# Optimization experiments

Hardware: AMD Instinct MI355X
Metric: run time of the kernel (lower is better)

Reference implementation:

```python
import jax, jax.numpy as jnp
import numpy as np
from jax import lax

ALPHA = 0.02


def setup_inputs() -> dict:
    key = jax.random.key(0)
    k1, k2, k3, k4 = jax.random.split(key, 4)
    B, C, H, W = 32, 512, 64, 64
    Cr = C // 16  # reduction=16
    x = jax.random.normal(k1, (B, C, H, W), dtype=jnp.float32)
    w1 = jax.random.normal(k2, (Cr, C), dtype=jnp.float32) * 0.05  # Linear(C -> C/r), bias=False
    w2 = jax.random.normal(k3, (C, Cr), dtype=jnp.float32) * 0.05  # Linear(C/r -> C), bias=False
    wconv = jax.random.normal(k4, (1, 2, 7, 7), dtype=jnp.float32) * 0.05  # Conv2d(2,1,7,pad=3)
    return {"x": x, "w1": w1, "w2": w2, "wconv": wconv}


def _mlp(v, w1, w2):
    # shared MLP: Linear -> ReLU -> Linear (no biases)
    return jax.nn.relu(v @ w1.T) @ w2.T


def reference(x, w1, w2, wconv):
    # Channel attention: global avg and max pooling over H,W -> [B, C]
    avg = jnp.mean(x, axis=(2, 3))
    maxv = jnp.max(x, axis=(2, 3))
    mc = jax.nn.sigmoid(_mlp(avg, w1, w2) + _mlp(maxv, w1, w2))[:, :, None, None]  # [B,C,1,1]

    # Spatial attention: mean/max over channels -> [B, 2, H, W], then 7x7 conv
    xs = jnp.concatenate(
        [jnp.mean(x, axis=1, keepdims=True), jnp.max(x, axis=1, keepdims=True)], axis=1
    )
    ms = jax.nn.sigmoid(
        lax.conv_general_dilated(
            xs, wconv, window_strides=(1, 1), padding=[(3, 3), (3, 3)],
            dimension_numbers=("NCHW", "OIHW", "NCHW"),
        )
    )  # [B,1,H,W]

    # Soft gating with alpha blending, residual_scale=0 so output is x * att
    att = (1.0 - ALPHA + ALPHA * mc) * (1.0 - ALPHA + ALPHA * ms)
    return x * att
```

## Files before the change

kernel.cpp:

```cpp
#include <hip/hip_runtime.h>
#include <math.h>

#define ALPHA_F 0.02f

constexpr int Bn  = 32;
constexpr int Cn  = 512;
constexpr int CRn = 32;
constexpr int HWn = 4096;
constexpr int NCG = 8;
constexpr int NPG = 4;

__device__ __forceinline__ float sigmoidf_(float v) {
    return 1.0f / (1.0f + expf(-v));
}

__global__ __launch_bounds__(256) void k1_reduce(
    const float* __restrict__ x,
    float* __restrict__ cps, float* __restrict__ cpm,
    float* __restrict__ sps, float* __restrict__ spm)
{
    const int bid = blockIdx.x;
    const int pg  = bid & 3;
    const int cg  = (bid >> 2) & 7;
    const int b   = bid >> 5;
    const int t    = threadIdx.x;
    const int wv   = t >> 6;
    const int lane = t & 63;

    __shared__ float ls[4][1024];
    __shared__ float lm[4][1024];

    const float* xb = x + ((size_t)b * Cn + (size_t)cg * 64) * HWn + pg * 1024;

    float4 psum[4], pmax[4];
#pragma unroll
    for (int q = 0; q < 4; ++q) {
        psum[q] = make_float4(0.f, 0.f, 0.f, 0.f);
        pmax[q] = make_float4(-INFINITY, -INFINITY, -INFINITY, -INFINITY);
    }

#pragma unroll 4
    for (int cl = 0; cl < 16; ++cl) {
        const int c = wv * 16 + cl;
        const float4* row = (const float4*)(xb + (size_t)c * HWn);
        float lsum = 0.f, lmax = -INFINITY;
#pragma unroll
        for (int q = 0; q < 4; ++q) {
            const float4 v = row[q * 64 + lane];
            psum[q].x += v.x; psum[q].y += v.y; psum[q].z += v.z; psum[q].w += v.w;
            pmax[q].x = fmaxf(pmax[q].x, v.x);
            pmax[q].y = fmaxf(pmax[q].y, v.y);
            pmax[q].z = fmaxf(pmax[q].z, v.z);
            pmax[q].w = fmaxf(pmax[q].w, v.w);
            lsum += (v.x + v.y) + (v.z + v.w);
            lmax = fmaxf(lmax, fmaxf(fmaxf(v.x, v.y), fmaxf(v.z, v.w)));
        }
#pragma unroll
        for (int m = 32; m >= 1; m >>= 1) {
            lsum += __shfl_xor(lsum, m, 64);
            lmax = fmaxf(lmax, __shfl_xor(lmax, m, 64));
        }
        if (lane == 0) {
            const int cglob = cg * 64 + c;
            cps[(pg * Bn + b) * Cn + cglob] = lsum;
            cpm[(pg * Bn + b) * Cn + cglob] = lmax;
        }
    }

    float4* lsw = (float4*)ls[wv];
    float4* lmw = (float4*)lm[wv];
#pragma unroll
    for (int q = 0; q < 4; ++q) {
        lsw[q * 64 + lane] = psum[q];
        lmw[q * 64 + lane] = pmax[q];
    }
    __syncthreads();

    float4 s  = ((const float4*)ls[0])[t];
    float4 mx = ((const float4*)lm[0])[t];
#pragma unroll
    for (int w = 1; w < 4; ++w) {
        const float4 a  = ((const float4*)ls[w])[t];
        const float4 bb = ((const float4*)lm[w])[t];
        s.x += a.x; s.y += a.y; s.z += a.z; s.w += a.w;
        mx.x = fmaxf(mx.x, bb.x); mx.y = fmaxf(mx.y, bb.y);
        mx.z = fmaxf(mx.z, bb.z); mx.w = fmaxf(mx.w, bb.w);
    }
    float4* os = (float4*)(sps + ((size_t)cg * Bn + b) * HWn + pg * 1024);
    float4* om = (float4*)(spm + ((size_t)cg * Bn + b) * HWn + pg * 1024);
    os[t] = s;
    om[t] = mx;
}

__global__ __launch_bounds__(256) void k2_spatial_finalize(
    const float* __restrict__ sps, const float* __restrict__ spm,
    float* __restrict__ savg, float* __restrict__ smax)
{
    const int i = blockIdx.x * 256 + threadIdx.x;
    const float4* ps = (const float4*)sps;
    const float4* pm = (const float4*)spm;
    float4 s = ps[i], m = pm[i];
#pragma unroll
    for (int cg = 1; cg < NCG; ++cg) {
        const float4 a  = ps[cg * (Bn * HWn / 4) + i];
        const float4 b4 = pm[cg * (Bn * HWn / 4) + i];
        s.x += a.x; s.y += a.y; s.z += a.z; s.w += a.w;
        m.x = fmaxf(m.x, b4.x); m.y = fmaxf(m.y, b4.y);
        m.z = fmaxf(m.z, b4.z); m.w = fmaxf(m.w, b4.w);
    }
    const float inv = 1.0f / (float)Cn;
    s.x *= inv; s.y *= inv; s.z *= inv; s.w *= inv;
    ((float4*)savg)[i] = s;
    ((float4*)smax)[i] = m;
}

__global__ __launch_bounds__(256) void k2_mlp(
    const float* __restrict__ cps, const float* __restrict__ cpm,
    const float* __restrict__ w1, const float* __restrict__ w2,
    float* __restrict__ mcF)
{
    const int b = blockIdx.x;
    const int t = threadIdx.x;
    __shared__ float avg[Cn];
    __shared__ float mxv[Cn];
    __shared__ float hs[CRn];

    for (int c = t; c < Cn; c += 256) {
        float s = 0.f, m = -INFINITY;
#pragma unroll
        for (int pgi = 0; pgi < NPG; ++pgi) {
            s += cps[(pgi * Bn + b) * Cn + c];
            m = fmaxf(m, cpm[(pgi * Bn + b) * Cn + c]);
        }
        avg[c] = s * (1.0f / (float)HWn);
        mxv[c] = m;
    }
    __syncthreads();

    const int j = t >> 3, s8 = t & 7;
    float pa = 0.f, pm = 0.f;
    const float* w1r = w1 + j * Cn + s8 * 64;
    const float* av  = avg + s8 * 64;
    const float* mv  = mxv + s8 * 64;
    for (int k = 0; k < 64; ++k) {
        pa += av[k] * w1r[k];
        pm += mv[k] * w1r[k];
    }
    pa += __shfl_xor(pa, 1, 64); pm += __shfl_xor(pm, 1, 64);
    pa += __shfl_xor(pa, 2, 64); pm += __shfl_xor(pm, 2, 64);
    pa += __shfl_xor(pa, 4, 64); pm += __shfl_xor(pm, 4, 64);
    if (s8 == 0) hs[j] = fmaxf(pa, 0.f) + fmaxf(pm, 0.f);
    __syncthreads();

    for (int c = t; c < Cn; c += 256) {
        float o = 0.f;
        const float* w2r = w2 + c * CRn;
#pragma unroll
        for (int jj = 0; jj < CRn; ++jj) o += hs[jj] * w2r[jj];
        mcF[b * Cn + c] = 1.0f - ALPHA_F + ALPHA_F * sigmoidf_(o);
    }
}

__global__ __launch_bounds__(256) void k3_conv(
    const float* __restrict__ savg, const float* __restrict__ smax,
    const float* __restrict__ wconv, float* __restrict__ msF)
{
    __shared__ float wc[98];
    const int t = threadIdx.x;
    if (t < 98) wc[t] = wconv[t];
    __syncthreads();

    const int p  = blockIdx.x * 256 + t;
    const int b  = p >> 12;
    const int pl = p & 4095;
    const int y  = pl >> 6, xc = pl & 63;
    const float* sa = savg + b * HWn;
    const float* sm = smax + b * HWn;
    float acc = 0.f;
#pragma unroll
    for (int ky = 0; ky < 7; ++ky) {
        const int yy = y + ky - 3;
        if (yy < 0 || yy >= 64) continue;
#pragma unroll
        for (int kx = 0; kx < 7; ++kx) {
            const int xx = xc + kx - 3;
            if (xx < 0 || xx >= 64) continue;
            const int off = (yy << 6) + xx;
            acc += wc[ky * 7 + kx] * sa[off] + wc[49 + ky * 7 + kx] * sm[off];
        }
    }
    msF[p] = 1.0f - ALPHA_F + ALPHA_F * sigmoidf_(acc);
}

__global__ __launch_bounds__(256) void k4_apply(
    const float* __restrict__ x, const float* __restrict__ mcF,
    const float* __restrict__ msF, float* __restrict__ out)
{
    const long long N4 = (long long)Bn * Cn * HWn / 4;
    const long long stride = (long long)gridDim.x * 256;
    const float4* x4  = (const float4*)x;
    const float4* ms4 = (const float4*)msF;
    float4* o4 = (float4*)out;
    for (long long v = (long long)blockIdx.x * 256 + threadIdx.x; v < N4; v += stride) {
        const int bc = (int)(v >> 10);
        const int pq = (int)(v & 1023);
        const int b  = bc >> 9;
        const float f = mcF[bc];
        const float4 m = ms4[b * 1024 + pq];
        float4 xv = x4[v];
        xv.x *= f * m.x; xv.y *= f * m.y; xv.z *= f * m.z; xv.w *= f * m.w;
        o4[v] = xv;
    }
}

extern "C" void kernel_launch(void* const* d_in, const int* in_sizes, int n_in,
                              void* d_out, int out_size, void* d_ws, size_t ws_size,
                              hipStream_t stream)
{
    const float* x     = (const float*)d_in[0];
    const float* w1    = (const float*)d_in[1];
    const float* w2    = (const float*)d_in[2];
    const float* wconv = (const float*)d_in[3];
    float* out = (float*)d_out;

    float* p = (float*)d_ws;
    float* cps  = p; p += NPG * Bn * Cn;
    float* cpm  = p; p += NPG * Bn * Cn;
    float* sps  = p; p += NCG * Bn * HWn;
    float* spm  = p; p += NCG * Bn * HWn;
    float* savg = p; p += Bn * HWn;
    float* smax = p; p += Bn * HWn;
    float* mcF  = p; p += Bn * Cn;
    float* msF  = p; p += Bn * HWn;

    hipLaunchKernelGGL(k1_reduce, dim3(Bn * NCG * NPG), dim3(256), 0, stream,
                       x, cps, cpm, sps, spm);
    hipLaunchKernelGGL(k2_spatial_finalize, dim3(Bn * HWn / 4 / 256), dim3(256), 0, stream,
                       sps, spm, savg, smax);
    hipLaunchKernelGGL(k2_mlp, dim3(Bn), dim3(256), 0, stream,
                       cps, cpm, w1, w2, mcF);
    hipLaunchKernelGGL(k3_conv, dim3(Bn * HWn / 256), dim3(256), 0, stream,
                       savg, smax, wconv, msF);
    hipLaunchKernelGGL(k4_apply, dim3(4096), dim3(256), 0, stream,
                       x, mcF, msF, out);
}
```

Before: 182.1 us.

## Fuse spatial finalize, MLP and conv into one per-batch kernel; nontemporal output stores

Merges the spatial channel-group reduction, the channel MLP and the 7x7 conv into a single kernel with one block per batch. The reduced avg/max maps stay in shared memory instead of going through global buffers. This removes two kernel launches and the global round trip of the intermediate maps. The cost is that the middle stage now runs on only 32 blocks, each doing serial work over 4096 pixels. Separately, the apply kernel uses vector-type arithmetic and nontemporal stores for the output.

```diff
diff --git a/kernel.cpp b/kernel.cpp
--- a/kernel.cpp
+++ b/kernel.cpp
@@ -9,6 +9,8 @@
 constexpr int HWn = 4096;
 constexpr int NCG = 8;
 constexpr int NPG = 4;
+
+typedef float floatx4 __attribute__((ext_vector_type(4)));
 
 __device__ __forceinline__ float sigmoidf_(float v) {
     return 1.0f / (1.0f + expf(-v));
@@ -92,38 +94,46 @@
     om[t] = mx;
 }
 
-__global__ __launch_bounds__(256) void k2_spatial_finalize(
+__global__ __launch_bounds__(256) void k2_mid(
     const float* __restrict__ sps, const float* __restrict__ spm,
-    float* __restrict__ savg, float* __restrict__ smax)
-{
-    const int i = blockIdx.x * 256 + threadIdx.x;
-    const float4* ps = (const float4*)sps;
-    const float4* pm = (const float4*)spm;
-    float4 s = ps[i], m = pm[i];
-#pragma unroll
-    for (int cg = 1; cg < NCG; ++cg) {
-        const float4 a  = ps[cg * (Bn * HWn / 4) + i];
-        const float4 b4 = pm[cg * (Bn * HWn / 4) + i];
-        s.x += a.x; s.y += a.y; s.z += a.z; s.w += a.w;
-        m.x = fmaxf(m.x, b4.x); m.y = fmaxf(m.y, b4.y);
-        m.z = fmaxf(m.z, b4.z); m.w = fmaxf(m.w, b4.w);
-    }
-    const float inv = 1.0f / (float)Cn;
-    s.x *= inv; s.y *= inv; s.z *= inv; s.w *= inv;
-    ((float4*)savg)[i] = s;
-    ((float4*)smax)[i] = m;
-}
-
-__global__ __launch_bounds__(256) void k2_mlp(
     const float* __restrict__ cps, const float* __restrict__ cpm,
     const float* __restrict__ w1, const float* __restrict__ w2,
-    float* __restrict__ mcF)
+    const float* __restrict__ wconv,
+    float* __restrict__ mcF, float* __restrict__ msF)
 {
     const int b = blockIdx.x;
     const int t = threadIdx.x;
+
+    __shared__ float sa[HWn];
+    __shared__ float sm[HWn];
     __shared__ float avg[Cn];
     __shared__ float mxv[Cn];
     __shared__ float hs[CRn];
+    __shared__ float wc[98];
+    if (t < 98) wc[t] = wconv[t];
+
+    {
+        const float4* ps = (const float4*)sps + (size_t)b * 1024;
+        const float4* pm = (const float4*)spm + (size_t)b * 1024;
+        const int cgstep = Bn * 1024;
+        const float inv = 1.0f / (float)Cn;
+#pragma unroll
+        for (int k = 0; k < 4; ++k) {
+            const int i = t + 256 * k;
+            float4 s = ps[i], m = pm[i];
+#pragma unroll
+            for (int cg = 1; cg < NCG; ++cg) {
+                const float4 a  = ps[cg * cgstep + i];
+                const float4 b4 = pm[cg * cgstep + i];
+                s.x += a.x; s.y += a.y; s.z += a.z; s.w += a.w;
+                m.x = fmaxf(m.x, b4.x); m.y = fmaxf(m.y, b4.y);
+                m.z = fmaxf(m.z, b4.z); m.w = fmaxf(m.w, b4.w);
+            }
+            s.x *= inv; s.y *= inv; s.z *= inv; s.w *= inv;
+            ((float4*)sa)[i] = s;
+            ((float4*)sm)[i] = m;
+        }
+    }
 
     for (int c = t; c < Cn; c += 256) {
         float s = 0.f, m = -INFINITY;
@@ -138,18 +148,18 @@
     __syncthreads();
 
     const int j = t >> 3, s8 = t & 7;
-    float pa = 0.f, pm = 0.f;
+    float pa = 0.f, pm2 = 0.f;
     const float* w1r = w1 + j * Cn + s8 * 64;
     const float* av  = avg + s8 * 64;
     const float* mv  = mxv + s8 * 64;
     for (int k = 0; k < 64; ++k) {
-        pa += av[k] * w1r[k];
-        pm += mv[k] * w1r[k];
-    }
-    pa += __shfl_xor(pa, 1, 64); pm += __shfl_xor(pm, 1, 64);
-    pa += __shfl_xor(pa, 2, 64); pm += __shfl_xor(pm, 2, 64);
-    pa += __shfl_xor(pa, 4, 64); pm += __shfl_xor(pm, 4, 64);
-    if (s8 == 0) hs[j] = fmaxf(pa, 0.f) + fmaxf(pm, 0.f);
+        pa  += av[k] * w1r[k];
+        pm2 += mv[k] * w1r[k];
+    }
+    pa += __shfl_xor(pa, 1, 64); pm2 += __shfl_xor(pm2, 1, 64);
+    pa += __shfl_xor(pa, 2, 64); pm2 += __shfl_xor(pm2, 2, 64);
+    pa += __shfl_xor(pa, 4, 64); pm2 += __shfl_xor(pm2, 4, 64);
+    if (s8 == 0) hs[j] = fmaxf(pa, 0.f) + fmaxf(pm2, 0.f);
     __syncthreads();
 
     for (int c = t; c < Cn; c += 256) {
@@ -159,37 +169,26 @@
         for (int jj = 0; jj < CRn; ++jj) o += hs[jj] * w2r[jj];
         mcF[b * Cn + c] = 1.0f - ALPHA_F + ALPHA_F * sigmoidf_(o);
     }
-}
-
-__global__ __launch_bounds__(256) void k3_conv(
-    const float* __restrict__ savg, const float* __restrict__ smax,
-    const float* __restrict__ wconv, float* __restrict__ msF)
-{
-    __shared__ float wc[98];
-    const int t = threadIdx.x;
-    if (t < 98) wc[t] = wconv[t];
-    __syncthreads();
-
-    const int p  = blockIdx.x * 256 + t;
-    const int b  = p >> 12;
-    const int pl = p & 4095;
-    const int y  = pl >> 6, xc = pl & 63;
-    const float* sa = savg + b * HWn;
-    const float* sm = smax + b * HWn;
-    float acc = 0.f;
-#pragma unroll
-    for (int ky = 0; ky < 7; ++ky) {
-        const int yy = y + ky - 3;
-        if (yy < 0 || yy >= 64) continue;
-#pragma unroll
-        for (int kx = 0; kx < 7; ++kx) {
-            const int xx = xc + kx - 3;
-            if (xx < 0 || xx >= 64) continue;
-            const int off = (yy << 6) + xx;
-            acc += wc[ky * 7 + kx] * sa[off] + wc[49 + ky * 7 + kx] * sm[off];
-        }
-    }
-    msF[p] = 1.0f - ALPHA_F + ALPHA_F * sigmoidf_(acc);
+
+#pragma unroll
+    for (int k = 0; k < 16; ++k) {
+        const int p = t + 256 * k;
+        const int y = p >> 6, xc = p & 63;
+        float acc = 0.f;
+#pragma unroll
+        for (int ky = 0; ky < 7; ++ky) {
+            const int yy = y + ky - 3;
+            if (yy < 0 || yy >= 64) continue;
+#pragma unroll
+            for (int kx = 0; kx < 7; ++kx) {
+                const int xx = xc + kx - 3;
+                if (xx < 0 || xx >= 64) continue;
+                const int off = (yy << 6) + xx;
+                acc += wc[ky * 7 + kx] * sa[off] + wc[49 + ky * 7 + kx] * sm[off];
+            }
+        }
+        msF[b * HWn + p] = 1.0f - ALPHA_F + ALPHA_F * sigmoidf_(acc);
+    }
 }
 
 __global__ __launch_bounds__(256) void k4_apply(
@@ -198,18 +197,18 @@
 {
     const long long N4 = (long long)Bn * Cn * HWn / 4;
     const long long stride = (long long)gridDim.x * 256;
-    const float4* x4  = (const float4*)x;
-    const float4* ms4 = (const float4*)msF;
-    float4* o4 = (float4*)out;
+    const floatx4* x4  = (const floatx4*)x;
+    const floatx4* ms4 = (const floatx4*)msF;
+    floatx4* o4 = (floatx4*)out;
     for (long long v = (long long)blockIdx.x * 256 + threadIdx.x; v < N4; v += stride) {
         const int bc = (int)(v >> 10);
         const int pq = (int)(v & 1023);
         const int b  = bc >> 9;
         const float f = mcF[bc];
-        const float4 m = ms4[b * 1024 + pq];
-        float4 xv = x4[v];
-        xv.x *= f * m.x; xv.y *= f * m.y; xv.z *= f * m.z; xv.w *= f * m.w;
-        o4[v] = xv;
+        const floatx4 m = ms4[b * 1024 + pq];
+        floatx4 xv = x4[v];
+        xv *= f * m;
+        __builtin_nontemporal_store(xv, &o4[v]);
     }
 }
 
@@ -228,19 +227,13 @@
     float* cpm  = p; p += NPG * Bn * Cn;
     float* sps  = p; p += NCG * Bn * HWn;
     float* spm  = p; p += NCG * Bn * HWn;
-    float* savg = p; p += Bn * HWn;
-    float* smax = p; p += Bn * HWn;
     float* mcF  = p; p += Bn * Cn;
     float* msF  = p; p += Bn * HWn;
 
     hipLaunchKernelGGL(k1_reduce, dim3(Bn * NCG * NPG), dim3(256), 0, stream,
                        x, cps, cpm, sps, spm);
-    hipLaunchKernelGGL(k2_spatial_finalize, dim3(Bn * HWn / 4 / 256), dim3(256), 0, stream,
-                       sps, spm, savg, smax);
-    hipLaunchKernelGGL(k2_mlp, dim3(Bn), dim3(256), 0, stream,
-                       cps, cpm, w1, w2, mcF);
-    hipLaunchKernelGGL(k3_conv, dim3(Bn * HWn / 256), dim3(256), 0, stream,
-                       savg, smax, wconv, msF);
+    hipLaunchKernelGGL(k2_mid, dim3(Bn), dim3(256), 0, stream,
+                       sps, spm, cps, cpm, w1, w2, wconv, mcF, msF);
     hipLaunchKernelGGL(k4_apply, dim3(4096), dim3(256), 0, stream,
                        x, mcF, msF, out);
 }
```

Measured after the change: 206.9 us. 13.6% more time.
